# Performance work log

Measured on AMD Instinct MI355X. Metric: run time of the kernel, lower is better.

Reference implementation:

```python
import jax, jax.numpy as jnp
import numpy as np

N_PARENTS = 4096   # parent clusters
K = 32             # points decoded per cluster
NEIGH = 128        # neigh_dec_size
FEAT = 256         # input_size (per-parent feature dim passed through)


def setup_inputs() -> dict:
    key = jax.random.key(0)
    ks = jax.random.split(key, 6)
    def lin(k, fan_in, fan_out):
        return jax.random.normal(k, (fan_in, fan_out), jnp.float32) / np.sqrt(fan_in).astype(np.float32)
    return {
        "input_features": jax.random.normal(ks[0], (N_PARENTS, NEIGH + FEAT), jnp.float32),
        # neighborhood decoder: Linear NEIGH -> K*3 (relative points)
        "W_dec": lin(ks[1], NEIGH, K * 3), "b_dec": jnp.zeros((K * 3,), jnp.float32),
        # fc chain: (FEAT+3) -> 512 -> 512 -> 256
        "W1": lin(ks[2], FEAT + 3, 512), "b1": jnp.zeros((512,), jnp.float32),
        "W2": lin(ks[3], 512, 512),      "b2": jnp.zeros((512,), jnp.float32),
        "W3": lin(ks[4], 512, 256),      "b3": jnp.zeros((256,), jnp.float32),
    }


def reference(input_features, W_dec, b_dec, W1, b1, W2, b2, W3, b3):
    # split: first NEIGH dims go to the neighborhood decoder, rest are parent features
    neigh_feats = input_features[:, :NEIGH]            # [N, NEIGH]
    features = input_features[:, NEIGH:]               # [N, FEAT]

    # neighborhood_dec: decode K relative 3D points per parent + cluster assignment
    relative_points = (neigh_feats @ W_dec + b_dec).reshape(-1, 3)   # [N*K, 3]
    cluster = jnp.repeat(jnp.arange(N_PARENTS, dtype=jnp.int32), K)  # [N*K]

    # gather parent features per point, concat with relative points
    features_dup = features[cluster]                                  # [N*K, FEAT]
    h = jnp.concatenate([features_dup, relative_points], axis=1)      # [N*K, FEAT+3]

    # chained Linear + ReLU (leaky=False)
    h = jax.nn.relu(h @ W1 + b1)
    h = jax.nn.relu(h @ W2 + b2)
    h = jax.nn.relu(h @ W3 + b3)
    return relative_points, h, cluster
```

## Files before the change

### kernel.cpp

```cpp
#include <hip/hip_runtime.h>
#include <hip/hip_bf16.h>

typedef unsigned short u16;
typedef unsigned int   u32;

#define NP     4096
#define NCH    131072
#define HBASE  393216
#define CLBASE 33947648

#define WS_W2F   0
#define WS_W3F   524288
#define WS_F1    1048576

using bf16x8 = __attribute__((ext_vector_type(8))) short;
using f32x4  = __attribute__((ext_vector_type(4))) float;

__device__ inline u32 pk2(float a, float b) {
  __hip_bfloat162 h = __float22bfloat162_rn(make_float2(a, b));
  return *reinterpret_cast<u32*>(&h);
}

__device__ inline int swz(int r, int cg) {
  return cg ^ (r & 7) ^ ((r >> 3) & 3);
}

__global__ __launch_bounds__(512, 2) void k_pre(const float* __restrict__ in_feats,
                                                const float* __restrict__ Wd,
                                                const float* __restrict__ bd,
                                                const float* __restrict__ W1,
                                                const float* __restrict__ b1,
                                                const float* __restrict__ W2,
                                                const float* __restrict__ W3,
                                                u16* __restrict__ w2f,
                                                u16* __restrict__ w3f,
                                                float* __restrict__ F1,
                                                float* __restrict__ out) {
  __shared__ __align__(16) char smem[69504];
  int b = blockIdx.x, tid = threadIdx.x;

  if (b < 256) {
    u16*   sh_a = (u16*)smem;
    float* b1s  = (float*)(smem + 8192);
    float* wdT  = (float*)(smem + 10240);
    float* ne   = (float*)(smem + 60928);
    float* bds  = (float*)(smem + 69120);
    int p0 = b * 16, lane = tid & 63, w = tid >> 6;
    b1s[tid] = b1[tid];
    if (tid < 96) bds[tid] = bd[tid];
    {
      int r = tid >> 5, k4 = (tid & 31) * 4;
      *(float4*)(ne + r * 128 + k4) = *(const float4*)(in_feats + (p0 + r) * 384 + k4);
    }
    {
      int r = tid >> 5, k0 = (tid & 31) * 8;
      const float4 v0 = *(const float4*)(in_feats + (p0 + r) * 384 + 128 + k0);
      const float4 v1 = *(const float4*)(in_feats + (p0 + r) * 384 + 128 + k0 + 4);
      uint4 o;
      o.x = pk2(v0.x, v0.y); o.y = pk2(v0.z, v0.w);
      o.z = pk2(v1.x, v1.y); o.w = pk2(v1.z, v1.w);
      int slot = (k0 >> 3) ^ (r & 7);
      *(uint4*)(sh_a + r * 256 + slot * 8) = o;
    }
    {
#pragma unroll
      for (int i = 0; i < 6; ++i) {
        int idx = i * 512 + tid;
        int k = idx / 24, c4 = (idx % 24) * 4;
        const float4 v = *(const float4*)(Wd + k * 96 + c4);
        wdT[(c4 + 0) * 132 + k] = v.x;
        wdT[(c4 + 1) * 132 + k] = v.y;
        wdT[(c4 + 2) * 132 + k] = v.z;
        wdT[(c4 + 3) * 132 + k] = v.w;
      }
    }
    __syncthreads();
#pragma unroll
    for (int j = 0; j < 3; ++j) {
      int u = j * 512 + tid;
      int p = u / 96, c = u - p * 96;
      const float4* nep = (const float4*)(ne + p * 128);
      const float4* wp  = (const float4*)(wdT + c * 132);
      float4 a4 = {0.f, 0.f, 0.f, 0.f};
#pragma unroll 8
      for (int kq = 0; kq < 32; ++kq) {
        const float4 av = nep[kq], bv = wp[kq];
        a4.x += av.x * bv.x; a4.y += av.y * bv.y;
        a4.z += av.z * bv.z; a4.w += av.w * bv.w;
      }
      out[(p0 + p) * 96 + c] = bds[c] + ((a4.x + a4.y) + (a4.z + a4.w));
    }
    f32x4 acc[4];
#pragma unroll
    for (int i = 0; i < 4; ++i) acc[i] = f32x4{0.f, 0.f, 0.f, 0.f};
    int col = lane & 15, q8 = (lane >> 4) * 8;
#pragma unroll
    for (int kc = 0; kc < 8; ++kc) {
      int slot = ((kc * 32 + q8) >> 3) ^ (col & 7);
      bf16x8 a = *(const bf16x8*)(sh_a + col * 256 + slot * 8);
#pragma unroll
      for (int nf = 0; nf < 4; ++nf) {
        const float* wp = W1 + (kc * 32 + q8) * 512 + (w * 4 + nf) * 16 + col;
        float v0 = wp[0],      v1 = wp[512],  v2 = wp[1024], v3 = wp[1536];
        float v4 = wp[2048],   v5 = wp[2560], v6 = wp[3072], v7 = wp[3584];
        union { bf16x8 v; u32 u[4]; } uu;
        uu.u[0] = pk2(v0, v1); uu.u[1] = pk2(v2, v3);
        uu.u[2] = pk2(v4, v5); uu.u[3] = pk2(v6, v7);
        acc[nf] = __builtin_amdgcn_mfma_f32_16x16x32_bf16(a, uu.v, acc[nf], 0, 0, 0);
      }
    }
    int rb = (lane >> 4) * 4;
#pragma unroll
    for (int nf = 0; nf < 4; ++nf) {
      int n = w * 64 + nf * 16 + col;
#pragma unroll
      for (int i = 0; i < 4; ++i)
        F1[(p0 + rb + i) * 512 + n] = acc[nf][i] + b1s[n];
    }
  } else if (b < 448) {
    float (*tile)[32][33] = (float (*)[32][33])smem;
    int h = tid >> 8, t = tid & 255;
    const float* src; u16* dst; int pitchN, g;
    if (b < 384) { g = (b - 256) * 2 + h; src = W2; dst = w2f; pitchN = 512; }
    else         { g = (b - 384) * 2 + h; src = W3; dst = w3f; pitchN = 256; }
    int kt = g & 15, nt = g >> 4;
    {
      int kk = t >> 3, n4 = (t & 7) * 4;
      const float4 v = *(const float4*)(src + (kt * 32 + kk) * pitchN + nt * 32 + n4);
      tile[h][kk][n4 + 0] = v.x; tile[h][kk][n4 + 1] = v.y;
      tile[h][kk][n4 + 2] = v.z; tile[h][kk][n4 + 3] = v.w;
    }
    __syncthreads();
    {
      int s = t >> 1, half = t & 1, fr = s >> 6, l = s & 63;
      int n_l = fr * 16 + (l & 15);
      int k_l = (l >> 4) * 8 + half * 4;
      uint2 o;
      o.x = pk2(tile[h][k_l + 0][n_l], tile[h][k_l + 1][n_l]);
      o.y = pk2(tile[h][k_l + 2][n_l], tile[h][k_l + 3][n_l]);
      int frag_id = (nt * 2 + fr) * 16 + kt;
      *(uint2*)(dst + frag_id * 512 + l * 8 + half * 4) = o;
    }
  } else {
    int idx = ((b - 448) * 512 + tid) * 4;
    float c = (float)(idx >> 5);
    float* p = out + CLBASE + idx;
    __builtin_nontemporal_store(c, p + 0);
    __builtin_nontemporal_store(c, p + 1);
    __builtin_nontemporal_store(c, p + 2);
    __builtin_nontemporal_store(c, p + 3);
  }
}

__global__ __launch_bounds__(1024) void k_main(const float* __restrict__ W1,
                                               const float* __restrict__ b2,
                                               const float* __restrict__ b3,
                                               const u16* __restrict__ w2f,
                                               const u16* __restrict__ w3f,
                                               const float* __restrict__ F1,
                                               float* __restrict__ out) {
  int blk = blockIdx.x;
  int tid = threadIdx.x, lane = tid & 63, w = tid >> 6;
  int wm = w >> 3, wn = w & 7;
  int col = lane & 15, q = lane >> 4, q8 = q * 8;
  __shared__ u16 sh_h[128 * 512];
  __shared__ float f1s[2048], w1bs[1536], b2s[512], b3s[256], rels[384];

  if (tid < 512) *(float4*)(f1s + tid * 4) = *(const float4*)(F1 + blk * 2048 + tid * 4);
  if (tid < 768) *(float2*)(w1bs + tid * 2) = *(const float2*)(W1 + 131072 + tid * 2);
  if (tid < 512) b2s[tid] = b2[tid];
  if (tid >= 512 && tid < 768) b3s[tid - 512] = b3[tid - 512];
  if (tid >= 768 && tid < 1024) {
    float2 rv = *(const float2*)(out + blk * 384 + (tid - 768) * 2);
    rels[(tid - 768) * 2 + 0] = rv.x;
    rels[(tid - 768) * 2 + 1] = rv.y;
  }
  __syncthreads();

  {
    int row = tid >> 3, g = tid & 7, pp = row >> 5;
    float r0 = rels[row * 3 + 0], r1 = rels[row * 3 + 1], r2 = rels[row * 3 + 2];
#pragma unroll
    for (int j = 0; j < 8; ++j) {
      int c8 = g * 8 + j * 64;
      const float4 fa = *(const float4*)(f1s + pp * 512 + c8);
      const float4 fb = *(const float4*)(f1s + pp * 512 + c8 + 4);
      const float4 wa0 = *(const float4*)(w1bs + c8);
      const float4 wb0 = *(const float4*)(w1bs + c8 + 4);
      const float4 wa1 = *(const float4*)(w1bs + 512 + c8);
      const float4 wb1 = *(const float4*)(w1bs + 512 + c8 + 4);
      const float4 wa2 = *(const float4*)(w1bs + 1024 + c8);
      const float4 wb2 = *(const float4*)(w1bs + 1024 + c8 + 4);
      float v0 = fmaxf(fa.x + r0 * wa0.x + r1 * wa1.x + r2 * wa2.x, 0.f);
      float v1 = fmaxf(fa.y + r0 * wa0.y + r1 * wa1.y + r2 * wa2.y, 0.f);
      float v2 = fmaxf(fa.z + r0 * wa0.z + r1 * wa1.z + r2 * wa2.z, 0.f);
      float v3 = fmaxf(fa.w + r0 * wa0.w + r1 * wa1.w + r2 * wa2.w, 0.f);
      float v4 = fmaxf(fb.x + r0 * wb0.x + r1 * wb1.x + r2 * wb2.x, 0.f);
      float v5 = fmaxf(fb.y + r0 * wb0.y + r1 * wb1.y + r2 * wb2.y, 0.f);
      float v6 = fmaxf(fb.z + r0 * wb0.z + r1 * wb1.z + r2 * wb2.z, 0.f);
      float v7 = fmaxf(fb.w + r0 * wb0.w + r1 * wb1.w + r2 * wb2.w, 0.f);
      uint4 o;
      o.x = pk2(v0, v1); o.y = pk2(v2, v3);
      o.z = pk2(v4, v5); o.w = pk2(v6, v7);
      *(uint4*)(sh_h + row * 512 + swz(row, c8 >> 3) * 8) = o;
    }
  }
  __syncthreads();

  f32x4 acc2[4][4];
#pragma unroll
  for (int mf = 0; mf < 4; ++mf)
#pragma unroll
    for (int nf = 0; nf < 4; ++nf) acc2[mf][nf] = f32x4{0.f, 0.f, 0.f, 0.f};
  {
    const u16* w2p = w2f + (size_t)(wn * 4 * 16) * 512 + lane * 8;
    bf16x8 bufA[4], bufB[4];
#pragma unroll
    for (int nf = 0; nf < 4; ++nf) bufA[nf] = *(const bf16x8*)(w2p + nf * 16 * 512);
#pragma unroll 2
    for (int kc = 0; kc < 16; ++kc) {
      const bf16x8* cur = (kc & 1) ? bufB : bufA;
      bf16x8* nxt = (kc & 1) ? bufA : bufB;
      if (kc < 15) {
#pragma unroll
        for (int nf = 0; nf < 4; ++nf)
          nxt[nf] = *(const bf16x8*)(w2p + (nf * 16 + kc + 1) * 512);
      }
      int cb = (kc * 32 + q8) >> 3;
#pragma unroll
      for (int mf = 0; mf < 4; ++mf) {
        int r = wm * 64 + mf * 16 + col;
        bf16x8 a = *(const bf16x8*)(sh_h + r * 512 + swz(r, cb) * 8);
#pragma unroll
        for (int nf = 0; nf < 4; ++nf)
          acc2[mf][nf] = __builtin_amdgcn_mfma_f32_16x16x32_bf16(a, cur[nf], acc2[mf][nf], 0, 0, 0);
      }
    }
  }
  __syncthreads();

  {
    int rq = q * 4;
#pragma unroll
    for (int mf = 0; mf < 4; ++mf)
#pragma unroll
      for (int nf = 0; nf < 4; ++nf) {
        int n = wn * 64 + nf * 16 + col, cg = n >> 3, n7 = n & 7;
        float bv = b2s[n];
#pragma unroll
        for (int i = 0; i < 4; i += 2) {
          int r0 = wm * 64 + mf * 16 + rq + i, r1 = r0 + 1;
          u32 p = pk2(fmaxf(acc2[mf][nf][i] + bv, 0.f),
                      fmaxf(acc2[mf][nf][i + 1] + bv, 0.f));
          sh_h[r0 * 512 + swz(r0, cg) * 8 + n7] = (u16)(p & 0xffff);
          sh_h[r1 * 512 + swz(r1, cg) * 8 + n7] = (u16)(p >> 16);
        }
      }
  }
  __syncthreads();

  f32x4 acc3[4][2];
#pragma unroll
  for (int mf = 0; mf < 4; ++mf)
#pragma unroll
    for (int nf = 0; nf < 2; ++nf) acc3[mf][nf] = f32x4{0.f, 0.f, 0.f, 0.f};
  {
    const u16* w3p = w3f + (size_t)(wn * 2 * 16) * 512 + lane * 8;
    bf16x8 bufA[2], bufB[2];
#pragma unroll
    for (int nf = 0; nf < 2; ++nf) bufA[nf] = *(const bf16x8*)(w3p + nf * 16 * 512);
#pragma unroll 2
    for (int kc = 0; kc < 16; ++kc) {
      const bf16x8* cur = (kc & 1) ? bufB : bufA;
      bf16x8* nxt = (kc & 1) ? bufA : bufB;
      if (kc < 15) {
#pragma unroll
        for (int nf = 0; nf < 2; ++nf)
          nxt[nf] = *(const bf16x8*)(w3p + (nf * 16 + kc + 1) * 512);
      }
      int cb = (kc * 32 + q8) >> 3;
#pragma unroll
      for (int mf = 0; mf < 4; ++mf) {
        int r = wm * 64 + mf * 16 + col;
        bf16x8 a = *(const bf16x8*)(sh_h + r * 512 + swz(r, cb) * 8);
#pragma unroll
        for (int nf = 0; nf < 2; ++nf)
          acc3[mf][nf] = __builtin_amdgcn_mfma_f32_16x16x32_bf16(a, cur[nf], acc3[mf][nf], 0, 0, 0);
      }
    }
  }

  {
    int rq = q * 4;
#pragma unroll
    for (int mf = 0; mf < 4; ++mf)
#pragma unroll
      for (int nf = 0; nf < 2; ++nf) {
        int n = wn * 32 + nf * 16 + col;
        float bv = b3s[n];
#pragma unroll
        for (int i = 0; i < 4; ++i) {
          int r = wm * 64 + mf * 16 + rq + i;
          float v = fmaxf(acc3[mf][nf][i] + bv, 0.f);
          __builtin_nontemporal_store(v, out + HBASE + (blk * 128 + r) * 256 + n);
        }
      }
  }
}

extern "C" void kernel_launch(void* const* d_in, const int* in_sizes, int n_in,
                              void* d_out, int out_size, void* d_ws, size_t ws_size,
                              hipStream_t stream) {
  const float* in_feats = (const float*)d_in[0];
  const float* Wd = (const float*)d_in[1];
  const float* bd = (const float*)d_in[2];
  const float* W1 = (const float*)d_in[3];
  const float* b1 = (const float*)d_in[4];
  const float* W2 = (const float*)d_in[5];
  const float* b2 = (const float*)d_in[6];
  const float* W3 = (const float*)d_in[7];
  const float* b3 = (const float*)d_in[8];
  float* out = (float*)d_out;
  char* ws = (char*)d_ws;
  u16*   w2f = (u16*)(ws + WS_W2F);
  u16*   w3f = (u16*)(ws + WS_W3F);
  float* F1  = (float*)(ws + WS_F1);

  k_pre<<<512, 512, 0, stream>>>(in_feats, Wd, bd, W1, b1, W2, W3, w2f, w3f, F1, out);
  k_main<<<1024, 1024, 0, stream>>>(W1, b2, b3, w2f, w3f, F1, out);
}
```

Measured before the change: 267.1 us.

## Switch layer-2/3 GEMMs to 32x32x16 MFMA with repacked weight fragments

Replaces the 16x16x32 bf16 MFMA tiles in the W2 and W3 layers with 32x32x16 MFMA tiles, so each wave holds 2x2 (or 2x1) 32x32 accumulators. The weight pre-packing kernel is changed to emit fragments in the 32x32 operand layout, and the A-operand LDS reads and the epilogue row mapping are rewritten to match. The intent is fewer LDS A/B fragment loads per FLOP and higher MFMA throughput per instruction. It also trims the rels-load thread range so it no longer reads past the 384 floats. Register pressure rises with the 16-wide accumulators and the fully unrolled K loop.

```diff
diff --git a/kernel.cpp b/kernel.cpp
--- a/kernel.cpp
+++ b/kernel.cpp
@@ -15,6 +15,7 @@
 
 using bf16x8 = __attribute__((ext_vector_type(8))) short;
 using f32x4  = __attribute__((ext_vector_type(4))) float;
+using f32x16 = __attribute__((ext_vector_type(16))) float;
 
 __device__ inline u32 pk2(float a, float b) {
   __hip_bfloat162 h = __float22bfloat162_rn(make_float2(a, b));
@@ -132,13 +133,13 @@
     }
     __syncthreads();
     {
-      int s = t >> 1, half = t & 1, fr = s >> 6, l = s & 63;
-      int n_l = fr * 16 + (l & 15);
-      int k_l = (l >> 4) * 8 + half * 4;
+      int h2i = t >> 7, l = (t >> 1) & 63, half = t & 1;
+      int kk = h2i * 16 + (l >> 5) * 8 + half * 4;
+      int nn = l & 31;
       uint2 o;
-      o.x = pk2(tile[h][k_l + 0][n_l], tile[h][k_l + 1][n_l]);
-      o.y = pk2(tile[h][k_l + 2][n_l], tile[h][k_l + 3][n_l]);
-      int frag_id = (nt * 2 + fr) * 16 + kt;
+      o.x = pk2(tile[h][kk + 0][nn], tile[h][kk + 1][nn]);
+      o.y = pk2(tile[h][kk + 2][nn], tile[h][kk + 3][nn]);
+      int frag_id = nt * 32 + kt * 2 + h2i;
       *(uint2*)(dst + frag_id * 512 + l * 8 + half * 4) = o;
     }
   } else {
@@ -162,7 +163,7 @@
   int blk = blockIdx.x;
   int tid = threadIdx.x, lane = tid & 63, w = tid >> 6;
   int wm = w >> 3, wn = w & 7;
-  int col = lane & 15, q = lane >> 4, q8 = q * 8;
+  int r32 = lane & 31, kh = lane >> 5;
   __shared__ u16 sh_h[128 * 512];
   __shared__ float f1s[2048], w1bs[1536], b2s[512], b3s[256], rels[384];
 
@@ -170,7 +171,7 @@
   if (tid < 768) *(float2*)(w1bs + tid * 2) = *(const float2*)(W1 + 131072 + tid * 2);
   if (tid < 512) b2s[tid] = b2[tid];
   if (tid >= 512 && tid < 768) b3s[tid - 512] = b3[tid - 512];
-  if (tid >= 768 && tid < 1024) {
+  if (tid >= 768 && tid < 960) {
     float2 rv = *(const float2*)(out + blk * 384 + (tid - 768) * 2);
     rels[(tid - 768) * 2 + 0] = rv.x;
     rels[(tid - 768) * 2 + 1] = rv.y;
@@ -207,105 +208,110 @@
   }
   __syncthreads();
 
-  f32x4 acc2[4][4];
-#pragma unroll
-  for (int mf = 0; mf < 4; ++mf)
-#pragma unroll
-    for (int nf = 0; nf < 4; ++nf) acc2[mf][nf] = f32x4{0.f, 0.f, 0.f, 0.f};
-  {
-    const u16* w2p = w2f + (size_t)(wn * 4 * 16) * 512 + lane * 8;
-    bf16x8 bufA[4], bufB[4];
-#pragma unroll
-    for (int nf = 0; nf < 4; ++nf) bufA[nf] = *(const bf16x8*)(w2p + nf * 16 * 512);
-#pragma unroll 2
-    for (int kc = 0; kc < 16; ++kc) {
-      const bf16x8* cur = (kc & 1) ? bufB : bufA;
-      bf16x8* nxt = (kc & 1) ? bufA : bufB;
-      if (kc < 15) {
-#pragma unroll
-        for (int nf = 0; nf < 4; ++nf)
-          nxt[nf] = *(const bf16x8*)(w2p + (nf * 16 + kc + 1) * 512);
-      }
-      int cb = (kc * 32 + q8) >> 3;
-#pragma unroll
-      for (int mf = 0; mf < 4; ++mf) {
-        int r = wm * 64 + mf * 16 + col;
-        bf16x8 a = *(const bf16x8*)(sh_h + r * 512 + swz(r, cb) * 8);
-#pragma unroll
-        for (int nf = 0; nf < 4; ++nf)
-          acc2[mf][nf] = __builtin_amdgcn_mfma_f32_16x16x32_bf16(a, cur[nf], acc2[mf][nf], 0, 0, 0);
-      }
+  int arow0 = wm * 64 + r32, arow1 = arow0 + 32;
+  int ax0 = (arow0 & 7) ^ ((arow0 >> 3) & 3);
+  int ax1 = (arow1 & 7) ^ ((arow1 >> 3) & 3);
+  const u16* a0base = sh_h + arow0 * 512;
+  const u16* a1base = sh_h + arow1 * 512;
+
+#define LDA0(ks) (*(const bf16x8*)(a0base + ((((ks) * 2 + kh) ^ ax0) << 3)))
+#define LDA1(ks) (*(const bf16x8*)(a1base + ((((ks) * 2 + kh) ^ ax1) << 3)))
+
+  f32x16 acc2[2][2];
+#pragma unroll
+  for (int mt = 0; mt < 2; ++mt)
+#pragma unroll
+    for (int nt = 0; nt < 2; ++nt)
+#pragma unroll
+      for (int i = 0; i < 16; ++i) acc2[mt][nt][i] = 0.f;
+  {
+    const u16* w2p = w2f + (size_t)(wn * 2) * 32 * 512 + lane * 8;
+    bf16x8 A0[2], A1[2], B0[2], B1[2];
+    A0[0] = LDA0(0); A0[1] = LDA1(0);
+    B0[0] = *(const bf16x8*)(w2p);
+    B0[1] = *(const bf16x8*)(w2p + 32 * 512);
+#pragma unroll
+    for (int ks = 0; ks < 32; ks += 2) {
+      A1[0] = LDA0(ks + 1); A1[1] = LDA1(ks + 1);
+      B1[0] = *(const bf16x8*)(w2p + (ks + 1) * 512);
+      B1[1] = *(const bf16x8*)(w2p + (32 + ks + 1) * 512);
+      acc2[0][0] = __builtin_amdgcn_mfma_f32_32x32x16_bf16(A0[0], B0[0], acc2[0][0], 0, 0, 0);
+      acc2[0][1] = __builtin_amdgcn_mfma_f32_32x32x16_bf16(A0[0], B0[1], acc2[0][1], 0, 0, 0);
+      acc2[1][0] = __builtin_amdgcn_mfma_f32_32x32x16_bf16(A0[1], B0[0], acc2[1][0], 0, 0, 0);
+      acc2[1][1] = __builtin_amdgcn_mfma_f32_32x32x16_bf16(A0[1], B0[1], acc2[1][1], 0, 0, 0);
+      if (ks + 2 < 32) {
+        A0[0] = LDA0(ks + 2); A0[1] = LDA1(ks + 2);
+        B0[0] = *(const bf16x8*)(w2p + (ks + 2) * 512);
+        B0[1] = *(const bf16x8*)(w2p + (32 + ks + 2) * 512);
+      }
+      acc2[0][0] = __builtin_amdgcn_mfma_f32_32x32x16_bf16(A1[0], B1[0], acc2[0][0], 0, 0, 0);
+      acc2[0][1] = __builtin_amdgcn_mfma_f32_32x32x16_bf16(A1[0], B1[1], acc2[0][1], 0, 0, 0);
+      acc2[1][0] = __builtin_amdgcn_mfma_f32_32x32x16_bf16(A1[1], B1[0], acc2[1][0], 0, 0, 0);
+      acc2[1][1] = __builtin_amdgcn_mfma_f32_32x32x16_bf16(A1[1], B1[1], acc2[1][1], 0, 0, 0);
     }
   }
   __syncthreads();
 
   {
-    int rq = q * 4;
-#pragma unroll
-    for (int mf = 0; mf < 4; ++mf)
-#pragma unroll
-      for (int nf = 0; nf < 4; ++nf) {
-        int n = wn * 64 + nf * 16 + col, cg = n >> 3, n7 = n & 7;
+#pragma unroll
+    for (int mt = 0; mt < 2; ++mt)
+#pragma unroll
+      for (int nt = 0; nt < 2; ++nt) {
+        int n = wn * 64 + nt * 32 + r32, cg = n >> 3, n7 = n & 7;
         float bv = b2s[n];
 #pragma unroll
-        for (int i = 0; i < 4; i += 2) {
-          int r0 = wm * 64 + mf * 16 + rq + i, r1 = r0 + 1;
-          u32 p = pk2(fmaxf(acc2[mf][nf][i] + bv, 0.f),
-                      fmaxf(acc2[mf][nf][i + 1] + bv, 0.f));
-          sh_h[r0 * 512 + swz(r0, cg) * 8 + n7] = (u16)(p & 0xffff);
-          sh_h[r1 * 512 + swz(r1, cg) * 8 + n7] = (u16)(p >> 16);
+        for (int i = 0; i < 16; i += 2) {
+          int rin = (i & 3) + 8 * (i >> 2) + 4 * kh;
+          int ra = wm * 64 + mt * 32 + rin, rb = ra + 1;
+          u32 p = pk2(fmaxf(acc2[mt][nt][i] + bv, 0.f),
+                      fmaxf(acc2[mt][nt][i + 1] + bv, 0.f));
+          sh_h[ra * 512 + swz(ra, cg) * 8 + n7] = (u16)(p & 0xffff);
+          sh_h[rb * 512 + swz(rb, cg) * 8 + n7] = (u16)(p >> 16);
         }
       }
   }
   __syncthreads();
 
-  f32x4 acc3[4][2];
-#pragma unroll
-  for (int mf = 0; mf < 4; ++mf)
-#pragma unroll
-    for (int nf = 0; nf < 2; ++nf) acc3[mf][nf] = f32x4{0.f, 0.f, 0.f, 0.f};
-  {
-    const u16* w3p = w3f + (size_t)(wn * 2 * 16) * 512 + lane * 8;
-    bf16x8 bufA[2], bufB[2];
-#pragma unroll
-    for (int nf = 0; nf < 2; ++nf) bufA[nf] = *(const bf16x8*)(w3p + nf * 16 * 512);
-#pragma unroll 2
-    for (int kc = 0; kc < 16; ++kc) {
-      const bf16x8* cur = (kc & 1) ? bufB : bufA;
-      bf16x8* nxt = (kc & 1) ? bufA : bufB;
-      if (kc < 15) {
-#pragma unroll
-        for (int nf = 0; nf < 2; ++nf)
-          nxt[nf] = *(const bf16x8*)(w3p + (nf * 16 + kc + 1) * 512);
-      }
-      int cb = (kc * 32 + q8) >> 3;
-#pragma unroll
-      for (int mf = 0; mf < 4; ++mf) {
-        int r = wm * 64 + mf * 16 + col;
-        bf16x8 a = *(const bf16x8*)(sh_h + r * 512 + swz(r, cb) * 8);
-#pragma unroll
-        for (int nf = 0; nf < 2; ++nf)
-          acc3[mf][nf] = __builtin_amdgcn_mfma_f32_16x16x32_bf16(a, cur[nf], acc3[mf][nf], 0, 0, 0);
-      }
-    }
-  }
-
-  {
-    int rq = q * 4;
-#pragma unroll
-    for (int mf = 0; mf < 4; ++mf)
-#pragma unroll
-      for (int nf = 0; nf < 2; ++nf) {
-        int n = wn * 32 + nf * 16 + col;
-        float bv = b3s[n];
-#pragma unroll
-        for (int i = 0; i < 4; ++i) {
-          int r = wm * 64 + mf * 16 + rq + i;
-          float v = fmaxf(acc3[mf][nf][i] + bv, 0.f);
-          __builtin_nontemporal_store(v, out + HBASE + (blk * 128 + r) * 256 + n);
-        }
-      }
-  }
+  f32x16 acc3[2];
+#pragma unroll
+  for (int mt = 0; mt < 2; ++mt)
+#pragma unroll
+    for (int i = 0; i < 16; ++i) acc3[mt][i] = 0.f;
+  {
+    const u16* w3p = w3f + (size_t)(wn) * 32 * 512 + lane * 8;
+    bf16x8 A0[2], A1[2], B0, B1;
+    A0[0] = LDA0(0); A0[1] = LDA1(0);
+    B0 = *(const bf16x8*)(w3p);
+#pragma unroll
+    for (int ks = 0; ks < 32; ks += 2) {
+      A1[0] = LDA0(ks + 1); A1[1] = LDA1(ks + 1);
+      B1 = *(const bf16x8*)(w3p + (ks + 1) * 512);
+      acc3[0] = __builtin_amdgcn_mfma_f32_32x32x16_bf16(A0[0], B0, acc3[0], 0, 0, 0);
+      acc3[1] = __builtin_amdgcn_mfma_f32_32x32x16_bf16(A0[1], B0, acc3[1], 0, 0, 0);
+      if (ks + 2 < 32) {
+        A0[0] = LDA0(ks + 2); A0[1] = LDA1(ks + 2);
+        B0 = *(const bf16x8*)(w3p + (ks + 2) * 512);
+      }
+      acc3[0] = __builtin_amdgcn_mfma_f32_32x32x16_bf16(A1[0], B1, acc3[0], 0, 0, 0);
+      acc3[1] = __builtin_amdgcn_mfma_f32_32x32x16_bf16(A1[1], B1, acc3[1], 0, 0, 0);
+    }
+  }
+
+  {
+    int n = wn * 32 + r32;
+    float bv = b3s[n];
+#pragma unroll
+    for (int mt = 0; mt < 2; ++mt)
+#pragma unroll
+      for (int i = 0; i < 16; ++i) {
+        int rin = (i & 3) + 8 * (i >> 2) + 4 * kh;
+        int r = wm * 64 + mt * 32 + rin;
+        float v = fmaxf(acc3[mt][i] + bv, 0.f);
+        __builtin_nontemporal_store(v, out + HBASE + (blk * 128 + r) * 256 + n);
+      }
+  }
+#undef LDA0
+#undef LDA1
 }
 
 extern "C" void kernel_launch(void* const* d_in, const int* in_sizes, int n_in,
```

Result: no change. 266.2 us (-0.3%).
